# Kernel optimization log

Hardware: AMD Instinct MI355X
Metric: run time of the kernel (lower is better)

## Reference

```python
import jax, jax.numpy as jnp
import numpy as np

B, L, D, H = 1, 4096, 1024, 16
HD = D // H  # head dim = 64
WINDOW = 15


def _rope(t, cos, sin):
    # t: [B,H,L,HD]; cos/sin: [1,1,L,HD//2]
    tr = t.reshape(*t.shape[:-1], HD // 2, 2)
    a, b = tr[..., 0], tr[..., 1]
    out_r = a * cos - b * sin
    out_i = a * sin + b * cos
    return jnp.stack([out_r, out_i], axis=-1).reshape(t.shape)


def _longformer_mask(L, window):
    i = jnp.arange(L)[:, None]
    j = jnp.arange(L)[None, :]
    causal = j <= i
    win = jnp.abs(i - j) <= window // 2
    glob = (j == 0) | (i == 0)
    return (causal & win) | glob  # [L,L] bool


def setup_inputs() -> dict:
    key = jax.random.key(0)
    kx, kq, kk, kv, ko = jax.random.split(key, 5)
    x = jax.random.normal(kx, (B, L, D), dtype=jnp.float32)
    scale = 0.02
    Wq = jax.random.normal(kq, (D, D), dtype=jnp.float32) * scale
    Wk = jax.random.normal(kk, (D, D), dtype=jnp.float32) * scale
    Wv = jax.random.normal(kv, (D, D), dtype=jnp.float32) * scale
    Wo = jax.random.normal(ko, (D, D), dtype=jnp.float32) * scale
    # real RoPE frequencies (complex freqs_cis split into cos/sin)
    inv_freq = 1.0 / (10000.0 ** (np.arange(0, HD, 2, dtype=np.float32) / HD))
    pos = np.arange(L, dtype=np.float32)
    ang = pos[:, None] * inv_freq[None, :]  # [L, HD//2]
    freqs_cos = jnp.asarray(np.cos(ang))[None]  # [1,L,HD//2]
    freqs_sin = jnp.asarray(np.sin(ang))[None]
    return {"x": x, "Wq": Wq, "Wk": Wk, "Wv": Wv, "Wo": Wo,
            "freqs_cos": freqs_cos, "freqs_sin": freqs_sin}


def reference(x, Wq, Wk, Wv, Wo, freqs_cos, freqs_sin):
    b, l, _ = x.shape
    # projections (nn.Linear: y = x @ W^T)
    Q = (x @ Wq.T).reshape(b, l, H, HD).transpose(0, 2, 1, 3)  # [B,H,L,HD]
    K = (x @ Wk.T).reshape(b, l, H, HD).transpose(0, 2, 1, 3)
    V = (x @ Wv.T).reshape(b, l, H, HD).transpose(0, 2, 1, 3)
    cos = freqs_cos[:, None, :l]  # [1,1,L,HD//2] (torch unsqueeze(1))
    sin = freqs_sin[:, None, :l]
    Q = _rope(Q, cos, sin)
    K = _rope(K, cos, sin)
    mask = _longformer_mask(l, WINDOW)  # [L,L]
    scores = jnp.einsum('bhqd,bhkd->bhqk', Q, K) / jnp.sqrt(jnp.float32(HD))
    scores = jnp.where(mask[None, None], scores, jnp.finfo(scores.dtype).min)
    attn = jax.nn.softmax(scores, axis=-1)
    out = jnp.einsum('bhqk,bhkd->bhqd', attn, V)  # [B,H,L,HD]
    out = out.transpose(0, 2, 1, 3).reshape(b, l, D)
    return out @ Wo.T
```

## Files before the change

kernel.cpp:

```cpp
#include <hip/hip_runtime.h>
#include <stdint.h>

#define SL 4096
#define DM 1024
#define NH 16
#define HDIM 64

typedef short short8 __attribute__((ext_vector_type(8)));
typedef float f32x4 __attribute__((ext_vector_type(4)));

__device__ __forceinline__ unsigned short f2bf(float f) {
  unsigned int u = __float_as_uint(f);
  u += 0x7FFF + ((u >> 16) & 1);
  return (unsigned short)(u >> 16);
}
__device__ __forceinline__ float bf2f(unsigned short u) {
  return __uint_as_float((unsigned int)u << 16);
}
__device__ __forceinline__ float bflo(unsigned int u) { return __uint_as_float(u << 16); }
__device__ __forceinline__ float bfhi(unsigned int u) { return __uint_as_float(u & 0xffff0000u); }

__device__ __forceinline__ void gload_lds16(const void* g, void* l) {
  __builtin_amdgcn_global_load_lds((const __attribute__((address_space(1))) void*)g,
                                   (__attribute__((address_space(3))) void*)l, 16, 0, 0);
}

__global__ void cast4(const float* __restrict__ src, unsigned short* __restrict__ dst, int n4) {
  int i = blockIdx.x * blockDim.x + threadIdx.x;
  if (i >= n4) return;
  float4 v = ((const float4*)src)[i];
  ushort4 o = make_ushort4(f2bf(v.x), f2bf(v.y), f2bf(v.z), f2bf(v.w));
  ((ushort4*)dst)[i] = o;
}

__global__ void cast_weights(const float* __restrict__ Wq, const float* __restrict__ Wk,
                             const float* __restrict__ Wv, const float* __restrict__ Wo,
                             unsigned short* __restrict__ w3b, unsigned short* __restrict__ wob) {
  int i = blockIdx.x * blockDim.x + threadIdx.x;
  int seg = i >> 18;
  int off = i & 262143;
  const float* src = (seg == 0) ? Wq : (seg == 1) ? Wk : (seg == 2) ? Wv : Wo;
  unsigned short* dst = (seg < 3) ? (w3b + (size_t)seg * DM * DM) : wob;
  float4 v = ((const float4*)src)[off];
  ushort4 o = make_ushort4(f2bf(v.x), f2bf(v.y), f2bf(v.z), f2bf(v.w));
  ((ushort4*)dst)[off] = o;
}

template <bool BF16OUT, bool ROPE>
__global__ void gemm_bt(const unsigned short* __restrict__ A,
                        const unsigned short* __restrict__ B,
                        void* __restrict__ Cv,
                        int M, int N, int K, int ldc,
                        const float* __restrict__ fc, const float* __restrict__ fs) {
  __shared__ __align__(16) unsigned short As[2][128 * 32];
  __shared__ __align__(16) unsigned short Bs[2][128 * 32];
  const int tid  = threadIdx.x;
  const int w    = tid >> 6;
  const int lane = tid & 63;
  const int wr = w >> 1, wc = w & 1;
  const int brow = blockIdx.y * 128;
  const int bcol = blockIdx.x * 128;
  const int l4 = lane >> 2;
  const int lk = (lane & 3) * 8;
  const int lhalf = lane >> 4;
  const int lrow  = lane & 15;
  const int c0 = w * 2;

  const unsigned short* Ag0 = A + (size_t)(brow + c0 * 16 + l4) * K + lk;
  const unsigned short* Ag1 = A + (size_t)(brow + (c0 + 1) * 16 + l4) * K + lk;
  const unsigned short* Bg0 = B + (size_t)(bcol + c0 * 16 + l4) * K + lk;
  const unsigned short* Bg1 = B + (size_t)(bcol + (c0 + 1) * 16 + l4) * K + lk;

  f32x4 acc[4][4] = {};
  const int NT = K >> 5;

  auto STAGE = [&](int t, int b) {
    const int k0 = t << 5;
    gload_lds16(Ag0 + k0, &As[b][c0 * 512]);
    gload_lds16(Ag1 + k0, &As[b][(c0 + 1) * 512]);
    gload_lds16(Bg0 + k0, &Bs[b][c0 * 512]);
    gload_lds16(Bg1 + k0, &Bs[b][(c0 + 1) * 512]);
  };

  STAGE(0, 0);
  for (int t = 0; t < NT; ++t) {
    const int cur = t & 1;
    __syncthreads();
    if (t + 1 < NT) STAGE(t + 1, cur ^ 1);
    short8 af[4], bf[4];
#pragma unroll
    for (int m = 0; m < 4; ++m)
      af[m] = *(const short8*)&As[cur][(wr * 64 + m * 16 + lrow) * 32 + lhalf * 8];
#pragma unroll
    for (int n = 0; n < 4; ++n)
      bf[n] = *(const short8*)&Bs[cur][(wc * 64 + n * 16 + lrow) * 32 + lhalf * 8];
#pragma unroll
    for (int m = 0; m < 4; ++m)
#pragma unroll
      for (int n = 0; n < 4; ++n)
        acc[m][n] = __builtin_amdgcn_mfma_f32_16x16x32_bf16(af[m], bf[n], acc[m][n], 0, 0, 0);
  }

  const int er = (lane >> 4) * 4;
  const int ec = lane & 15;

  if constexpr (ROPE) {
    if (bcol + wc * 64 < 2048) {
#pragma unroll
      for (int n = 0; n < 4; ++n) {
        const int p = ((n * 16 + ec) & 63) >> 1;
#pragma unroll
        for (int m = 0; m < 4; ++m) {
#pragma unroll
          for (int r = 0; r < 4; ++r) {
            const int row = brow + wr * 64 + m * 16 + er + r;
            float v = acc[m][n][r];
            float pv = __shfl_xor(v, 1);
            float cs = fc[row * 32 + p], sn = fs[row * 32 + p];
            acc[m][n][r] = (lane & 1) ? (pv * sn + v * cs) : (v * cs - pv * sn);
          }
        }
      }
    }
  }

#pragma unroll
  for (int m = 0; m < 4; ++m)
#pragma unroll
    for (int n = 0; n < 4; ++n) {
      const size_t roff = (size_t)(brow + wr * 64 + m * 16 + er) * ldc + (bcol + wc * 64 + n * 16 + ec);
      if constexpr (BF16OUT) {
        unsigned short* cp = (unsigned short*)Cv + roff;
#pragma unroll
        for (int r = 0; r < 4; ++r) cp[(size_t)r * ldc] = f2bf(acc[m][n][r]);
      } else {
        float* cp = (float*)Cv + roff;
#pragma unroll
        for (int r = 0; r < 4; ++r) cp[(size_t)r * ldc] = acc[m][n][r];
      }
    }
}

__global__ __launch_bounds__(64)
void attn_row0_part(const unsigned short* __restrict__ qkv, float* __restrict__ prt) {
  const int p = blockIdx.x;
  const int h = blockIdx.y;
  const int lane = threadIdx.x;
  const float q = bf2f(qkv[h * 64 + lane]);
  float m = -1e30f, s = 0.f, o = 0.f;
  const int j0 = p * 32;
  for (int jj = 0; jj < 32; ++jj) {
    const int j = j0 + jj;
    float kv = bf2f(qkv[(size_t)j * 3072 + 1024 + h * 64 + lane]);
    float pr = q * kv;
#pragma unroll
    for (int off = 32; off; off >>= 1) pr += __shfl_xor(pr, off);
    pr *= 0.125f;
    float mn = fmaxf(m, pr);
    float c = __expf(m - mn);
    float e = __expf(pr - mn);
    float v = bf2f(qkv[(size_t)j * 3072 + 2048 + h * 64 + lane]);
    s = s * c + e;
    o = o * c + e * v;
    m = mn;
  }
  float* dst = prt + ((size_t)h * 128 + p) * 72;
  if (lane == 0) { dst[0] = m; dst[1] = s; }
  dst[2 + lane] = o;
}

__global__ __launch_bounds__(64)
void attn_row0_combine(const float* __restrict__ prt, unsigned short* __restrict__ atb) {
  const int h = blockIdx.x;
  const int lane = threadIdx.x;
  const float* base = prt + (size_t)h * 128 * 72;
  __shared__ float cbuf[128];
  float m0 = base[lane * 72];
  float m1 = base[(lane + 64) * 72];
  float M = fmaxf(m0, m1);
#pragma unroll
  for (int off = 32; off; off >>= 1) M = fmaxf(M, __shfl_xor(M, off));
  float c0 = __expf(m0 - M), c1 = __expf(m1 - M);
  float ls = base[lane * 72 + 1] * c0 + base[(lane + 64) * 72 + 1] * c1;
#pragma unroll
  for (int off = 32; off; off >>= 1) ls += __shfl_xor(ls, off);
  cbuf[lane] = c0;
  cbuf[lane + 64] = c1;
  __syncthreads();
  float o = 0.f;
#pragma unroll 8
  for (int p = 0; p < 128; ++p) o += cbuf[p] * base[p * 72 + 2 + lane];
  atb[h * 64 + lane] = f2bf(o / ls);
}

__global__ __launch_bounds__(256)
void attn_main(const unsigned short* __restrict__ qkv, unsigned short* __restrict__ atb) {
  const int i = blockIdx.x * 4 + (threadIdx.x >> 6) + 1;
  if (i >= SL) return;
  const int lane = threadIdx.x & 63;
  const unsigned short* rowQ = qkv + (size_t)i * 3072 + lane * 16;

  float q[16];
  {
    uint4 a = *(const uint4*)rowQ;
    uint4 b = *(const uint4*)(rowQ + 8);
    unsigned int uu[8] = {a.x, a.y, a.z, a.w, b.x, b.y, b.z, b.w};
#pragma unroll
    for (int c = 0; c < 8; ++c) { q[2 * c] = bflo(uu[c]); q[2 * c + 1] = bfhi(uu[c]); }
  }

  float sc[9];
#pragma unroll
  for (int t = 0; t < 9; ++t) {
    int j = (t == 0) ? 0 : (i - 8 + t);
    bool valid = (t == 0) || (j >= 1);
    int jc = valid ? j : 0;
    const unsigned short* pk = qkv + (size_t)jc * 3072 + 1024 + lane * 16;
    uint4 a = *(const uint4*)pk;
    uint4 b = *(const uint4*)(pk + 8);
    unsigned int uu[8] = {a.x, a.y, a.z, a.w, b.x, b.y, b.z, b.w};
    float pr = 0.f;
#pragma unroll
    for (int c = 0; c < 8; ++c) pr += bflo(uu[c]) * q[2 * c] + bfhi(uu[c]) * q[2 * c + 1];
    pr += __shfl_xor(pr, 1);
    pr += __shfl_xor(pr, 2);
    sc[t] = valid ? pr * 0.125f : -1e30f;
  }

  float mx = sc[0];
#pragma unroll
  for (int t = 1; t < 9; ++t) mx = fmaxf(mx, sc[t]);
  float s = 0.f;
#pragma unroll
  for (int t = 0; t < 9; ++t) { float e = __expf(sc[t] - mx); sc[t] = e; s += e; }
  const float inv = 1.0f / s;

  float o[16] = {};
#pragma unroll
  for (int t = 0; t < 9; ++t) {
    int j = (t == 0) ? 0 : (i - 8 + t);
    bool valid = (t == 0) || (j >= 1);
    int jc = valid ? j : 0;
    const unsigned short* pv = qkv + (size_t)jc * 3072 + 2048 + lane * 16;
    uint4 a = *(const uint4*)pv;
    uint4 b = *(const uint4*)(pv + 8);
    unsigned int uu[8] = {a.x, a.y, a.z, a.w, b.x, b.y, b.z, b.w};
#pragma unroll
    for (int c = 0; c < 8; ++c) {
      o[2 * c]     += sc[t] * bflo(uu[c]);
      o[2 * c + 1] += sc[t] * bfhi(uu[c]);
    }
  }

  unsigned int wv[8];
#pragma unroll
  for (int c = 0; c < 8; ++c)
    wv[c] = (unsigned int)f2bf(o[2 * c] * inv) | ((unsigned int)f2bf(o[2 * c + 1] * inv) << 16);
  unsigned short* po = atb + (size_t)i * 1024 + lane * 16;
  uint4 s0; s0.x = wv[0]; s0.y = wv[1]; s0.z = wv[2]; s0.w = wv[3];
  uint4 s1; s1.x = wv[4]; s1.y = wv[5]; s1.z = wv[6]; s1.w = wv[7];
  *(uint4*)po = s0;
  *(uint4*)(po + 8) = s1;
}

extern "C" void kernel_launch(void* const* d_in, const int* in_sizes, int n_in,
                              void* d_out, int out_size, void* d_ws, size_t ws_size,
                              hipStream_t stream) {
  const float* x  = (const float*)d_in[0];
  const float* Wq = (const float*)d_in[1];
  const float* Wk = (const float*)d_in[2];
  const float* Wv = (const float*)d_in[3];
  const float* Wo = (const float*)d_in[4];
  const float* fc = (const float*)d_in[5];
  const float* fs = (const float*)d_in[6];
  float* out = (float*)d_out;

  char* ws = (char*)d_ws;
  unsigned short* xb   = (unsigned short*)(ws);
  unsigned short* w3b  = (unsigned short*)(ws + ((size_t)8 << 20));
  unsigned short* wob  = (unsigned short*)(ws + ((size_t)14 << 20));
  unsigned short* qkvb = (unsigned short*)(ws + ((size_t)16 << 20));
  unsigned short* atb  = (unsigned short*)(ws + ((size_t)40 << 20));
  float*          prt  = (float*)(ws + ((size_t)48 << 20));

  cast4<<<(SL * DM / 4 + 255) / 256, 256, 0, stream>>>(x, xb, SL * DM / 4);
  cast_weights<<<(4 * DM * DM / 4) / 256, 256, 0, stream>>>(Wq, Wk, Wv, Wo, w3b, wob);

  dim3 g1(3072 / 128, SL / 128);
  gemm_bt<true, true><<<g1, 256, 0, stream>>>(xb, w3b, (void*)qkvb, SL, 3072, DM, 3072, fc, fs);

  attn_row0_part<<<dim3(128, NH), 64, 0, stream>>>(qkvb, prt);
  attn_row0_combine<<<NH, 64, 0, stream>>>(prt, atb);
  attn_main<<<1024, 256, 0, stream>>>(qkvb, atb);

  dim3 g2(DM / 128, SL / 128);
  gemm_bt<false, false><<<g2, 256, 0, stream>>>(atb, wob, (void*)out, SL, DM, DM, DM, nullptr, nullptr);
}
```

Measured before the change: 104.4 us.

## Triple-buffer GEMM LDS staging with partial vmcnt waits and XOR swizzle

Moves the bf16 GEMM from double to triple buffering in LDS. It keeps two tile loads in flight and waits with vmcnt(4) instead of a full barrier drain, so global-to-LDS loads overlap more with MFMA compute. It also XOR-swizzles the k-chunk offsets on both the global load and the LDS read side to reduce LDS bank conflicts. LDS use grows by half, which may lower occupancy. The hand-placed waitcnt depends on exactly four loads per stage, and at the second-to-last iteration no new loads are issued, so that wait may not cover the last stage's loads.

```diff
diff --git a/kernel.cpp b/kernel.cpp
--- a/kernel.cpp
+++ b/kernel.cpp
@@ -52,8 +52,8 @@
                         void* __restrict__ Cv,
                         int M, int N, int K, int ldc,
                         const float* __restrict__ fc, const float* __restrict__ fs) {
-  __shared__ __align__(16) unsigned short As[2][128 * 32];
-  __shared__ __align__(16) unsigned short Bs[2][128 * 32];
+  __shared__ __align__(16) unsigned short As[3][128 * 32];
+  __shared__ __align__(16) unsigned short Bs[3][128 * 32];
   const int tid  = threadIdx.x;
   const int w    = tid >> 6;
   const int lane = tid & 63;
@@ -61,15 +61,15 @@
   const int brow = blockIdx.y * 128;
   const int bcol = blockIdx.x * 128;
   const int l4 = lane >> 2;
-  const int lk = (lane & 3) * 8;
-  const int lhalf = lane >> 4;
-  const int lrow  = lane & 15;
+  const int lkS = (((lane & 3) ^ ((lane >> 3) & 3))) * 8;
+  const int lrow = lane & 15;
+  const int sw8 = (((lane >> 4) ^ ((lane >> 1) & 3))) * 8;
   const int c0 = w * 2;
 
-  const unsigned short* Ag0 = A + (size_t)(brow + c0 * 16 + l4) * K + lk;
-  const unsigned short* Ag1 = A + (size_t)(brow + (c0 + 1) * 16 + l4) * K + lk;
-  const unsigned short* Bg0 = B + (size_t)(bcol + c0 * 16 + l4) * K + lk;
-  const unsigned short* Bg1 = B + (size_t)(bcol + (c0 + 1) * 16 + l4) * K + lk;
+  const unsigned short* Ag0 = A + (size_t)(brow + c0 * 16 + l4) * K + lkS;
+  const unsigned short* Ag1 = A + (size_t)(brow + (c0 + 1) * 16 + l4) * K + lkS;
+  const unsigned short* Bg0 = B + (size_t)(bcol + c0 * 16 + l4) * K + lkS;
+  const unsigned short* Bg1 = B + (size_t)(bcol + (c0 + 1) * 16 + l4) * K + lkS;
 
   f32x4 acc[4][4] = {};
   const int NT = K >> 5;
@@ -81,25 +81,36 @@
     gload_lds16(Bg0 + k0, &Bs[b][c0 * 512]);
     gload_lds16(Bg1 + k0, &Bs[b][(c0 + 1) * 512]);
   };
-
-  STAGE(0, 0);
-  for (int t = 0; t < NT; ++t) {
-    const int cur = t & 1;
-    __syncthreads();
-    if (t + 1 < NT) STAGE(t + 1, cur ^ 1);
+  auto COMPUTE = [&](int cur) {
     short8 af[4], bf[4];
 #pragma unroll
     for (int m = 0; m < 4; ++m)
-      af[m] = *(const short8*)&As[cur][(wr * 64 + m * 16 + lrow) * 32 + lhalf * 8];
+      af[m] = *(const short8*)&As[cur][(wr * 64 + m * 16 + lrow) * 32 + sw8];
 #pragma unroll
     for (int n = 0; n < 4; ++n)
-      bf[n] = *(const short8*)&Bs[cur][(wc * 64 + n * 16 + lrow) * 32 + lhalf * 8];
+      bf[n] = *(const short8*)&Bs[cur][(wc * 64 + n * 16 + lrow) * 32 + sw8];
 #pragma unroll
     for (int m = 0; m < 4; ++m)
 #pragma unroll
       for (int n = 0; n < 4; ++n)
         acc[m][n] = __builtin_amdgcn_mfma_f32_16x16x32_bf16(af[m], bf[n], acc[m][n], 0, 0, 0);
-  }
+  };
+
+  STAGE(0, 0);
+  STAGE(1, 1);
+  for (int t = 0; t < NT - 1; ++t) {
+    asm volatile("s_waitcnt vmcnt(4)" ::: "memory");
+    __builtin_amdgcn_sched_barrier(0);
+    __builtin_amdgcn_s_barrier();
+    __builtin_amdgcn_sched_barrier(0);
+    if (t + 2 < NT) STAGE(t + 2, (t + 2) % 3);
+    COMPUTE(t % 3);
+  }
+  asm volatile("s_waitcnt vmcnt(0)" ::: "memory");
+  __builtin_amdgcn_sched_barrier(0);
+  __builtin_amdgcn_s_barrier();
+  __builtin_amdgcn_sched_barrier(0);
+  COMPUTE((NT - 1) % 3);
 
   const int er = (lane >> 4) * 4;
   const int ec = lane & 15;
```

Result: no change. 104.6 us (+0.2%).
